# Kernel optimization log

Measured on AMD Instinct MI355X. Metric: run time of the kernel, lower is better.

The kernel has to match this reference:

```python
import jax, jax.numpy as jnp
import numpy as np

HEADS = 7
DIM_HEAD = 64
SCALE = DIM_HEAD ** -0.5


def setup_inputs() -> dict:
    key = jax.random.key(0)
    ks = jax.random.split(key, 6)
    b, n, dim = 8, 1024, 448
    inner = HEADS * DIM_HEAD  # 448
    x = jax.random.normal(ks[0], (b, n, dim), dtype=jnp.float32)
    w_qv = jax.random.normal(ks[1], (dim, 2 * inner), dtype=jnp.float32) * 0.02
    ext_k = jax.random.normal(ks[2], (HEADS, n, DIM_HEAD), dtype=jnp.float32)
    ext_bias = jax.random.normal(ks[3], (HEADS, n, n), dtype=jnp.float32)
    w_out = jax.random.normal(ks[4], (inner, dim), dtype=jnp.float32) * 0.02
    b_out = jnp.zeros((dim,), dtype=jnp.float32)
    return {"x": x, "w_qv": w_qv, "ext_k": ext_k, "ext_bias": ext_bias,
            "w_out": w_out, "b_out": b_out}


def reference(x, w_qv, ext_k, ext_bias, w_out, b_out):
    b, n, dim = x.shape
    qv = x @ w_qv                                   # [b, n, 2*inner]
    q, v = jnp.split(qv, 2, axis=-1)
    # b n (h d) -> b h n d
    q = q.reshape(b, n, HEADS, DIM_HEAD).transpose(0, 2, 1, 3)
    v = v.reshape(b, n, HEADS, DIM_HEAD).transpose(0, 2, 1, 3)
    # scores vs external learned key, additive bias applied BEFORE scale
    dots = (jnp.einsum('bhnd,hmd->bhnm', q, ext_k) + ext_bias[None]) * SCALE
    attn = jax.nn.softmax(dots, axis=-1)
    out = jnp.einsum('bhnm,bhmd->bhnd', attn, v)
    out = out.transpose(0, 2, 1, 3).reshape(b, n, HEADS * DIM_HEAD)
    return out @ w_out + b_out  # dropout is identity in eval mode
```

## Files before the change

kernel.cpp:

```cpp
#include <hip/hip_runtime.h>
#include <hip/hip_bf16.h>
#include <hip/hip_fp16.h>

#define BATCH 8
#define NSEQ 1024
#define DIMM 448
#define NHEAD 7
#define HDIM 64
#define MROWS (BATCH*NSEQ)
#define KDIM 448
#define SCALE_F 0.125f

typedef short short8 __attribute__((ext_vector_type(8)));
typedef float floatx16 __attribute__((ext_vector_type(16)));

#define MFMA32(a,b,c) __builtin_amdgcn_mfma_f32_32x32x16_bf16(a,b,c,0,0,0)

__device__ __forceinline__ unsigned short f2bf(float f){
    __hip_bfloat16 h = __float2bfloat16(f);
    return *reinterpret_cast<unsigned short*>(&h);
}
__device__ __forceinline__ float bf2f(unsigned short u){
    __hip_bfloat16 h; *reinterpret_cast<unsigned short*>(&h) = u;
    return __bfloat162float(h);
}
__device__ __forceinline__ float h2f(unsigned short u){
    __half h; *reinterpret_cast<unsigned short*>(&h) = u;
    return __half2float(h);
}
__device__ __forceinline__ unsigned short f2h(float f){
    __half h = __float2half(f);
    return *reinterpret_cast<unsigned short*>(&h);
}

__global__ __launch_bounds__(256)
void prep_all(const float* __restrict__ x, const float* __restrict__ ek,
              const float* __restrict__ wqv, const float* __restrict__ wout,
              const float* __restrict__ eb,
              unsigned short* __restrict__ xh, unsigned short* __restrict__ ekh,
              unsigned short* __restrict__ wqvTh, unsigned short* __restrict__ woTh,
              unsigned short* __restrict__ woTl, unsigned short* __restrict__ bp)
{
    __shared__ float T[2][64][33];
    const int bx = blockIdx.x, tid = threadIdx.x;

    if (bx < 3584) {
        int i = bx*256 + tid;
        float4 v = ((const float4*)x)[i];
        ((ushort4*)xh)[i] = make_ushort4(f2bf(v.x), f2bf(v.y), f2bf(v.z), f2bf(v.w));
    } else if (bx < 4032) {
        int i = (bx-3584)*256 + tid;
        float4 v = ((const float4*)ek)[i];
        ((ushort4*)ekh)[i] = make_ushort4(f2bf(v.x), f2bf(v.y), f2bf(v.z), f2bf(v.w));
    } else if (bx < 4228) {
        int lid = (bx-4032)*4 + (tid>>6);
        int kc = lid % 56, ng = lid / 56;
        int n = ng*64 + (tid&63);
        unsigned short h[8];
#pragma unroll
        for (int j = 0; j < 8; ++j) h[j] = f2bf(wqv[(size_t)(kc*8+j)*896 + n]);
        size_t o = (size_t)n*KDIM + kc*8;
        *(ushort4*)(wqvTh + o)     = make_ushort4(h[0],h[1],h[2],h[3]);
        *(ushort4*)(wqvTh + o + 4) = make_ushort4(h[4],h[5],h[6],h[7]);
    } else if (bx < 4340) {
        int lid = (bx-4228)*4 + (tid>>6);
        int kc = lid % 56, ng = lid / 56;
        int n = ng*64 + (tid&63);
        ushort4 h0={0,0,0,0}, h1={0,0,0,0}, l0={0,0,0,0}, l1={0,0,0,0};
        if (n < DIMM) {
            unsigned short h[8], l[8];
#pragma unroll
            for (int j = 0; j < 8; ++j) {
                float f = wout[(size_t)(kc*8+j)*DIMM + n];
                h[j] = f2bf(f); l[j] = f2bf(f - bf2f(h[j]));
            }
            h0 = make_ushort4(h[0],h[1],h[2],h[3]); h1 = make_ushort4(h[4],h[5],h[6],h[7]);
            l0 = make_ushort4(l[0],l[1],l[2],l[3]); l1 = make_ushort4(l[4],l[5],l[6],l[7]);
        }
        size_t o = (size_t)n*KDIM + kc*8;
        *(ushort4*)(woTh + o) = h0; *(ushort4*)(woTh + o + 4) = h1;
        *(ushort4*)(woTl + o) = l0; *(ushort4*)(woTl + o + 4) = l1;
    } else {
        const int sub = tid >> 7, st = tid & 127;
        const int lid = (bx-4340)*2 + sub;
        const int mt = lid & 31, qt = (lid>>5) & 15, h = lid >> 9;
#pragma unroll
        for (int it = 0; it < 4; ++it) {
            int idx = it*128 + st;
            int row = idx >> 3, c4 = (idx & 7)*4;
            float4 v = *(const float4*)(eb + ((size_t)(h*NSEQ + qt*64 + row))*NSEQ + mt*32 + c4);
            T[sub][row][c4+0]=v.x; T[sub][row][c4+1]=v.y;
            T[sub][row][c4+2]=v.z; T[sub][row][c4+3]=v.w;
        }
        __syncthreads();
        const int g2 = st >> 6, lane = st & 63;
        const int lq = lane & 31, quad = lane >> 5;
        const int q = g2*32 + lq;
        unsigned short* dst = bp + ((((size_t)h*16 + qt)*32 + mt)*4 + g2*2)*512 + lane*8;
#pragma unroll
        for (int jj = 0; jj < 2; ++jj) {
            unsigned short o[8];
#pragma unroll
            for (int t = 0; t < 8; ++t) {
                int m = (t&3) + 8*(t>>2) + 16*jj + 4*quad;
                o[t] = f2h(T[sub][q][m] * SCALE_F);
            }
            *(ushort4*)(dst + jj*512)     = make_ushort4(o[0],o[1],o[2],o[3]);
            *(ushort4*)(dst + jj*512 + 4) = make_ushort4(o[4],o[5],o[6],o[7]);
        }
    }
}

__global__ __launch_bounds__(64, 2)
void gemm1_reg(const unsigned short* __restrict__ Ah, const unsigned short* __restrict__ Bh,
               unsigned short* __restrict__ qd, unsigned short* __restrict__ vTd)
{
    const int lane = threadIdx.x;
    const int lq = lane & 31, lh = lane >> 5;
    const int m0 = blockIdx.x * 64;
    const int y  = blockIdx.y;
    const int n0 = y * 64;
    const unsigned short* aB = Ah + (size_t)(m0 + lq)*KDIM + lh*8;
    const unsigned short* bB = Bh + (size_t)(n0 + lq)*KDIM + lh*8;

    floatx16 acc[2][2] = {};
    short8 aR[2][2][2], bR[2][2][2];
#define LD1(kt, par) {                                                        \
    _Pragma("unroll") for (int fm = 0; fm < 2; ++fm)                          \
    _Pragma("unroll") for (int c = 0; c < 2; ++c) {                           \
        aR[par][fm][c] = *(const short8*)(aB + (size_t)fm*32*KDIM + (kt)*32 + c*16); \
        bR[par][fm][c] = *(const short8*)(bB + (size_t)fm*32*KDIM + (kt)*32 + c*16); } }

    LD1(0, 0)
#pragma unroll
    for (int kt = 0; kt < 14; ++kt) {
        const int par = kt & 1;
        if (kt < 13) LD1(kt+1, par^1)
#pragma unroll
        for (int c = 0; c < 2; ++c)
#pragma unroll
            for (int fm = 0; fm < 2; ++fm)
#pragma unroll
                for (int fn = 0; fn < 2; ++fn)
                    acc[fm][fn] = MFMA32(aR[par][fm][c], bR[par][fn][c], acc[fm][fn]);
    }
#undef LD1

    if (y < NHEAD) {
#pragma unroll
        for (int fm = 0; fm < 2; ++fm)
#pragma unroll
            for (int fn = 0; fn < 2; ++fn) {
                const int d = fn*32 + lq;
#pragma unroll
                for (int r = 0; r < 16; ++r) {
                    const int gm = m0 + fm*32 + (r&3) + 8*(r>>2) + 4*lh;
                    const int b = gm >> 10, ns = gm & 1023;
                    qd[((size_t)((b*NHEAD + y)*NSEQ + ns))*HDIM + d] = f2bf(acc[fm][fn][r]);
                }
            }
    } else {
        const int head = y - NHEAD;
#pragma unroll
        for (int fm = 0; fm < 2; ++fm)
#pragma unroll
            for (int fn = 0; fn < 2; ++fn) {
                const int d = fn*32 + lq;
#pragma unroll
                for (int r = 0; r < 16; ++r) {
                    const int gm = m0 + fm*32 + (r&3) + 8*(r>>2) + 4*lh;
                    const int b = gm >> 10, ns = gm & 1023;
                    vTd[((size_t)((b*NHEAD + head)*HDIM + d))*NSEQ + ns] = f2bf(acc[fm][fn][r]);
                }
            }
    }
}

__global__ __launch_bounds__(64, 2)
void attn5(const unsigned short* __restrict__ qh_g, const unsigned short* __restrict__ vTh,
           const unsigned short* __restrict__ ekh, const unsigned short* __restrict__ bp,
           unsigned short* __restrict__ aoh, unsigned short* __restrict__ aol)
{
    __shared__ unsigned short pS[1024];
    __shared__ float linv[32];

    const int lane = threadIdx.x;
    const int lq = lane & 31, lh = lane >> 5;
    const int qt2 = blockIdx.x;
    const int qt = qt2 >> 1, g2 = qt2 & 1;
    const int head = blockIdx.y, b = blockIdx.z;
    const int bh = b*NHEAD + head;

    short8 qf[4];
#pragma unroll
    for (int c = 0; c < 4; ++c)
        qf[c] = *(const short8*)(qh_g +
            ((size_t)(bh*NSEQ) + qt2*32 + lq)*HDIM + c*16 + lh*8);

    const unsigned short* kB = ekh + ((size_t)head*NSEQ + lq)*HDIM + lh*8;
    const unsigned short* vB = vTh + ((size_t)(bh*HDIM) + lq)*NSEQ;
    const unsigned short* bB = bp + ((size_t)(head*16 + qt))*65536 + g2*1024 + lane*8;

    short8 kR[2][4], vR[2][4], bR[2][2];
#define PREF(J, par) { const int mm = ((J) < 32) ? (J) : 0;                    \
    _Pragma("unroll") for (int c = 0; c < 4; ++c)                              \
        kR[par][c] = *(const short8*)(kB + (size_t)mm*2048 + c*16);            \
    _Pragma("unroll") for (int c2 = 0; c2 < 2; ++c2)                           \
    _Pragma("unroll") for (int h2 = 0; h2 < 2; ++h2)                           \
        vR[par][c2*2+h2] = *(const short8*)(vB + (size_t)(h2*32)*NSEQ + mm*32 + (c2*2+lh)*8); \
    _Pragma("unroll") for (int u = 0; u < 2; ++u)                              \
        bR[par][u] = *(const short8*)(bB + ((size_t)mm*4 + u)*512); }

    floatx16 O[2] = {};
    float ls = 0.f;

#define SEC(J, par, nxt) {                                                     \
    PREF((J)+1, nxt)                                                           \
    floatx16 S = {};                                                           \
    _Pragma("unroll") for (int c = 0; c < 4; ++c)                              \
        S = MFMA32(kR[par][c], qf[c], S);                                      \
    _Pragma("unroll") for (int g = 0; g < 4; ++g) {                            \
        unsigned short hb[4];                                                  \
        _Pragma("unroll") for (int j2 = 0; j2 < 4; ++j2) {                     \
            const int i = g*4 + j2;                                            \
            float bs = h2f((unsigned short)bR[par][i>>3][i&7]);                \
            float pv = __expf(fmaf(S[i], SCALE_F, bs));                        \
            ls += pv;  hb[j2] = f2bf(pv);                                      \
        }                                                                      \
        *(ushort4*)(pS + g*256 + lq*8 + lh*4) = make_ushort4(hb[0],hb[1],hb[2],hb[3]); \
    }                                                                          \
    _Pragma("unroll") for (int c2 = 0; c2 < 2; ++c2) {                         \
        short8 pf = *(const short8*)(pS + ((c2*2+lh)*32 + lq)*8);              \
        O[0] = MFMA32(pf, vR[par][c2*2+0], O[0]);                              \
        O[1] = MFMA32(pf, vR[par][c2*2+1], O[1]);                              \
    } }

    PREF(0, 0)
    for (int jj = 0; jj < 16; ++jj) {
        SEC(2*jj,   0, 1)
        SEC(2*jj+1, 1, 0)
    }
#undef SEC
#undef PREF

    float lt = ls + __shfl_xor(ls, 32);
    if (lh == 0) linv[lq] = 1.f/lt;

#pragma unroll
    for (int r = 0; r < 16; ++r) {
        const int qr = (r&3) + 8*(r>>2) + 4*lh;
        const float inv = linv[qr];
        const size_t o = ((size_t)(b*NSEQ) + qt2*32 + qr)*DIMM + head*HDIM + lq;
        float v0 = O[0][r]*inv, v1 = O[1][r]*inv;
        unsigned short h0 = f2bf(v0), h1 = f2bf(v1);
        aoh[o]      = h0;  aol[o]      = f2bf(v0 - bf2f(h0));
        aoh[o + 32] = h1;  aol[o + 32] = f2bf(v1 - bf2f(h1));
    }
}

__global__ __launch_bounds__(64, 2)
void gemm2_reg(const unsigned short* __restrict__ Ah, const unsigned short* __restrict__ Al,
               const unsigned short* __restrict__ Bh, const unsigned short* __restrict__ Bl,
               const float* __restrict__ bias, float* __restrict__ out)
{
    const int lane = threadIdx.x;
    const int lq = lane & 31, lh = lane >> 5;
    const int m0 = blockIdx.x * 64;
    const int n0 = blockIdx.y * 64;
    const unsigned short* aBh = Ah + (size_t)(m0 + lq)*KDIM + lh*8;
    const unsigned short* aBl = Al + (size_t)(m0 + lq)*KDIM + lh*8;
    const unsigned short* bBh = Bh + (size_t)(n0 + lq)*KDIM + lh*8;
    const unsigned short* bBl = Bl + (size_t)(n0 + lq)*KDIM + lh*8;

    floatx16 acc[2][2] = {};
    short8 aH[2][2][2], aL[2][2][2], bH[2][2][2], bL[2][2][2];
#define LD2(kt, par) {                                                        \
    _Pragma("unroll") for (int fm = 0; fm < 2; ++fm)                          \
    _Pragma("unroll") for (int c = 0; c < 2; ++c) {                           \
        const size_t off = (size_t)fm*32*KDIM + (kt)*32 + c*16;               \
        aH[par][fm][c] = *(const short8*)(aBh + off);                         \
        aL[par][fm][c] = *(const short8*)(aBl + off);                         \
        bH[par][fm][c] = *(const short8*)(bBh + off);                         \
        bL[par][fm][c] = *(const short8*)(bBl + off); } }

    LD2(0, 0)
#pragma unroll
    for (int kt = 0; kt < 14; ++kt) {
        const int par = kt & 1;
        if (kt < 13) LD2(kt+1, par^1)
#pragma unroll
        for (int c = 0; c < 2; ++c)
#pragma unroll
            for (int fm = 0; fm < 2; ++fm)
#pragma unroll
                for (int fn = 0; fn < 2; ++fn) {
                    acc[fm][fn] = MFMA32(aH[par][fm][c], bH[par][fn][c], acc[fm][fn]);
                    acc[fm][fn] = MFMA32(aL[par][fm][c], bH[par][fn][c], acc[fm][fn]);
                    acc[fm][fn] = MFMA32(aH[par][fm][c], bL[par][fn][c], acc[fm][fn]);
                }
    }
#undef LD2

#pragma unroll
    for (int fm = 0; fm < 2; ++fm)
#pragma unroll
        for (int fn = 0; fn < 2; ++fn) {
            const int gn = n0 + fn*32 + lq;
            const float bv = bias[gn];
#pragma unroll
            for (int r = 0; r < 16; ++r) {
                const int gm = m0 + fm*32 + (r&3) + 8*(r>>2) + 4*lh;
                out[(size_t)gm*DIMM + gn] = acc[fm][fn][r] + bv;
            }
        }
}

extern "C" void kernel_launch(void* const* d_in, const int* in_sizes, int n_in,
                              void* d_out, int out_size, void* d_ws, size_t ws_size,
                              hipStream_t stream)
{
    const float* x    = (const float*)d_in[0];
    const float* wqv  = (const float*)d_in[1];
    const float* ek   = (const float*)d_in[2];
    const float* eb   = (const float*)d_in[3];
    const float* wout = (const float*)d_in[4];
    const float* bout = (const float*)d_in[5];
    float* out = (float*)d_out;

    const size_t MK = (size_t)MROWS*KDIM;
    const size_t EK = (size_t)NHEAD*NSEQ*HDIM;
    unsigned short* p = (unsigned short*)d_ws;
    unsigned short* xh    = p;  p += MK;
    unsigned short* wqvTh = p;  p += (size_t)896*KDIM;
    unsigned short* woTh  = p;  p += (size_t)512*KDIM;
    unsigned short* woTl  = p;  p += (size_t)512*KDIM;
    unsigned short* ekh   = p;  p += EK;
    unsigned short* qh    = p;  p += MK;
    unsigned short* vTh   = p;  p += MK;
    unsigned short* bp    = p;  p += (size_t)NHEAD*NSEQ*NSEQ;
    unsigned short* aoh   = p;  p += MK;
    unsigned short* aol   = p;  p += MK;

    prep_all<<<6132, 256, 0, stream>>>(x, ek, wqv, wout, eb,
                                       xh, ekh, wqvTh, woTh, woTl, bp);
    gemm1_reg<<<dim3(128, 14), 64, 0, stream>>>(xh, wqvTh, qh, vTh);
    attn5<<<dim3(32, NHEAD, BATCH), 64, 0, stream>>>(qh, vTh, ekh, bp, aoh, aol);
    gemm2_reg<<<dim3(128, 7), 64, 0, stream>>>(aoh, aol, woTh, woTl, bout, out);
}
```

Measured before the change: 221.1 us.

## Fold scale and log2e into Q and bias, use fp32 bias as MFMA init

Prescales Q and the external bias by scale*log2(e) so scores feed exp2 directly, and stores the bias in fp32 in MFMA fragment layout so it seeds the score accumulator instead of being added per element. The attention kernel becomes 4-wave blocks, one wave per batch sharing a head and query tile, with a swizzled block order so the bias tile is reused across batches in cache. This removes the per-element fp16 decode and FMA, but doubles the bias storage and read bandwidth.

```diff
diff --git a/kernel.cpp b/kernel.cpp
--- a/kernel.cpp
+++ b/kernel.cpp
@@ -10,6 +10,7 @@
 #define MROWS (BATCH*NSEQ)
 #define KDIM 448
 #define SCALE_F 0.125f
+#define QB_SC 0.18033688011112042f
 
 typedef short short8 __attribute__((ext_vector_type(8)));
 typedef float floatx16 __attribute__((ext_vector_type(16)));
@@ -23,14 +24,6 @@
 __device__ __forceinline__ float bf2f(unsigned short u){
     __hip_bfloat16 h; *reinterpret_cast<unsigned short*>(&h) = u;
     return __bfloat162float(h);
-}
-__device__ __forceinline__ float h2f(unsigned short u){
-    __half h; *reinterpret_cast<unsigned short*>(&h) = u;
-    return __half2float(h);
-}
-__device__ __forceinline__ unsigned short f2h(float f){
-    __half h = __float2half(f);
-    return *reinterpret_cast<unsigned short*>(&h);
 }
 
 __global__ __launch_bounds__(256)
@@ -39,9 +32,9 @@
               const float* __restrict__ eb,
               unsigned short* __restrict__ xh, unsigned short* __restrict__ ekh,
               unsigned short* __restrict__ wqvTh, unsigned short* __restrict__ woTh,
-              unsigned short* __restrict__ woTl, unsigned short* __restrict__ bp)
-{
-    __shared__ float T[2][64][33];
+              unsigned short* __restrict__ woTl, float* __restrict__ bp32)
+{
+    __shared__ float T[4][32][33];
     const int bx = blockIdx.x, tid = threadIdx.x;
 
     if (bx < 3584) {
@@ -81,33 +74,29 @@
         *(ushort4*)(woTh + o) = h0; *(ushort4*)(woTh + o + 4) = h1;
         *(ushort4*)(woTl + o) = l0; *(ushort4*)(woTl + o + 4) = l1;
     } else {
-        const int sub = tid >> 7, st = tid & 127;
-        const int lid = (bx-4340)*2 + sub;
-        const int mt = lid & 31, qt = (lid>>5) & 15, h = lid >> 9;
-#pragma unroll
-        for (int it = 0; it < 4; ++it) {
-            int idx = it*128 + st;
-            int row = idx >> 3, c4 = (idx & 7)*4;
-            float4 v = *(const float4*)(eb + ((size_t)(h*NSEQ + qt*64 + row))*NSEQ + mt*32 + c4);
-            T[sub][row][c4+0]=v.x; T[sub][row][c4+1]=v.y;
-            T[sub][row][c4+2]=v.z; T[sub][row][c4+3]=v.w;
+        const int su = tid >> 6, lane = tid & 63;
+        const int lid = (bx-4340)*4 + su;
+        const int mt = lid & 31, qt2 = (lid>>5) & 31, h = lid >> 10;
+        const int qr = lane >> 1, hf = lane & 1;
+        const float* src = eb + ((size_t)(h*NSEQ) + qt2*32 + qr)*NSEQ + mt*32 + hf*16;
+#pragma unroll
+        for (int j = 0; j < 4; ++j) {
+            float4 v = *(const float4*)(src + j*4);
+            T[su][qr][hf*16 + j*4+0] = v.x;  T[su][qr][hf*16 + j*4+1] = v.y;
+            T[su][qr][hf*16 + j*4+2] = v.z;  T[su][qr][hf*16 + j*4+3] = v.w;
         }
         __syncthreads();
-        const int g2 = st >> 6, lane = st & 63;
         const int lq = lane & 31, quad = lane >> 5;
-        const int q = g2*32 + lq;
-        unsigned short* dst = bp + ((((size_t)h*16 + qt)*32 + mt)*4 + g2*2)*512 + lane*8;
-#pragma unroll
-        for (int jj = 0; jj < 2; ++jj) {
-            unsigned short o[8];
-#pragma unroll
-            for (int t = 0; t < 8; ++t) {
-                int m = (t&3) + 8*(t>>2) + 16*jj + 4*quad;
-                o[t] = f2h(T[sub][q][m] * SCALE_F);
-            }
-            *(ushort4*)(dst + jj*512)     = make_ushort4(o[0],o[1],o[2],o[3]);
-            *(ushort4*)(dst + jj*512 + 4) = make_ushort4(o[4],o[5],o[6],o[7]);
+        float* dst = bp32 + ((size_t)((h*32 + qt2)*32 + mt))*1024 + lane*16;
+        float o[16];
+#pragma unroll
+        for (int r = 0; r < 16; ++r) {
+            const int m = (r&3) + 8*(r>>2) + 4*quad;
+            o[r] = T[su][lq][m] * QB_SC;
         }
+#pragma unroll
+        for (int u = 0; u < 4; ++u)
+            *(float4*)(dst + u*4) = make_float4(o[u*4],o[u*4+1],o[u*4+2],o[u*4+3]);
     }
 }
 
@@ -156,7 +145,7 @@
                 for (int r = 0; r < 16; ++r) {
                     const int gm = m0 + fm*32 + (r&3) + 8*(r>>2) + 4*lh;
                     const int b = gm >> 10, ns = gm & 1023;
-                    qd[((size_t)((b*NHEAD + y)*NSEQ + ns))*HDIM + d] = f2bf(acc[fm][fn][r]);
+                    qd[((size_t)((b*NHEAD + y)*NSEQ + ns))*HDIM + d] = f2bf(acc[fm][fn][r] * QB_SC);
                 }
             }
     } else {
@@ -176,19 +165,22 @@
     }
 }
 
-__global__ __launch_bounds__(64, 2)
-void attn5(const unsigned short* __restrict__ qh_g, const unsigned short* __restrict__ vTh,
-           const unsigned short* __restrict__ ekh, const unsigned short* __restrict__ bp,
+__global__ __launch_bounds__(256, 2)
+void attn8(const unsigned short* __restrict__ qh_g, const unsigned short* __restrict__ vTh,
+           const unsigned short* __restrict__ ekh, const float* __restrict__ bp32,
            unsigned short* __restrict__ aoh, unsigned short* __restrict__ aol)
 {
-    __shared__ unsigned short pS[1024];
-    __shared__ float linv[32];
-
-    const int lane = threadIdx.x;
+    __shared__ unsigned short pS[4][1024];
+    __shared__ float linv[4][32];
+
+    const int tid = threadIdx.x;
+    const int w = tid >> 6, lane = tid & 63;
     const int lq = lane & 31, lh = lane >> 5;
-    const int qt2 = blockIdx.x;
-    const int qt = qt2 >> 1, g2 = qt2 & 1;
-    const int head = blockIdx.y, b = blockIdx.z;
+
+    const int orig = blockIdx.x;
+    const int wg = (orig & 7)*56 + (orig >> 3);
+    const int bq = wg & 1, qt2 = (wg >> 1) & 31, head = wg >> 6;
+    const int b = bq*4 + w;
     const int bh = b*NHEAD + head;
 
     short8 qf[4];
@@ -199,38 +191,42 @@
 
     const unsigned short* kB = ekh + ((size_t)head*NSEQ + lq)*HDIM + lh*8;
     const unsigned short* vB = vTh + ((size_t)(bh*HDIM) + lq)*NSEQ;
-    const unsigned short* bB = bp + ((size_t)(head*16 + qt))*65536 + g2*1024 + lane*8;
-
-    short8 kR[2][4], vR[2][4], bR[2][2];
+    const float* bB = bp32 + ((size_t)(head*32 + qt2))*32768 + lane*16;
+
+    short8 kR[2][4], vR[2][4];
+    float4 bR[2][4];
 #define PREF(J, par) { const int mm = ((J) < 32) ? (J) : 0;                    \
     _Pragma("unroll") for (int c = 0; c < 4; ++c)                              \
         kR[par][c] = *(const short8*)(kB + (size_t)mm*2048 + c*16);            \
     _Pragma("unroll") for (int c2 = 0; c2 < 2; ++c2)                           \
     _Pragma("unroll") for (int h2 = 0; h2 < 2; ++h2)                           \
         vR[par][c2*2+h2] = *(const short8*)(vB + (size_t)(h2*32)*NSEQ + mm*32 + (c2*2+lh)*8); \
-    _Pragma("unroll") for (int u = 0; u < 2; ++u)                              \
-        bR[par][u] = *(const short8*)(bB + ((size_t)mm*4 + u)*512); }
+    _Pragma("unroll") for (int u = 0; u < 4; ++u)                              \
+        bR[par][u] = *(const float4*)(bB + (size_t)mm*1024 + u*4); }
 
     floatx16 O[2] = {};
     float ls = 0.f;
 
 #define SEC(J, par, nxt) {                                                     \
     PREF((J)+1, nxt)                                                           \
-    floatx16 S = {};                                                           \
+    floatx16 S;                                                                \
+    _Pragma("unroll") for (int u = 0; u < 4; ++u) {                            \
+        S[u*4+0] = bR[par][u].x; S[u*4+1] = bR[par][u].y;                      \
+        S[u*4+2] = bR[par][u].z; S[u*4+3] = bR[par][u].w;                      \
+    }                                                                          \
     _Pragma("unroll") for (int c = 0; c < 4; ++c)                              \
         S = MFMA32(kR[par][c], qf[c], S);                                      \
     _Pragma("unroll") for (int g = 0; g < 4; ++g) {                            \
         unsigned short hb[4];                                                  \
         _Pragma("unroll") for (int j2 = 0; j2 < 4; ++j2) {                     \
             const int i = g*4 + j2;                                            \
-            float bs = h2f((unsigned short)bR[par][i>>3][i&7]);                \
-            float pv = __expf(fmaf(S[i], SCALE_F, bs));                        \
+            float pv = __builtin_amdgcn_exp2f(S[i]);                           \
             ls += pv;  hb[j2] = f2bf(pv);                                      \
         }                                                                      \
-        *(ushort4*)(pS + g*256 + lq*8 + lh*4) = make_ushort4(hb[0],hb[1],hb[2],hb[3]); \
+        *(ushort4*)(pS[w] + g*256 + lq*8 + lh*4) = make_ushort4(hb[0],hb[1],hb[2],hb[3]); \
     }                                                                          \
     _Pragma("unroll") for (int c2 = 0; c2 < 2; ++c2) {                         \
-        short8 pf = *(const short8*)(pS + ((c2*2+lh)*32 + lq)*8);              \
+        short8 pf = *(const short8*)(pS[w] + ((c2*2+lh)*32 + lq)*8);           \
         O[0] = MFMA32(pf, vR[par][c2*2+0], O[0]);                              \
         O[1] = MFMA32(pf, vR[par][c2*2+1], O[1]);                              \
     } }
@@ -244,12 +240,12 @@
 #undef PREF
 
     float lt = ls + __shfl_xor(ls, 32);
-    if (lh == 0) linv[lq] = 1.f/lt;
+    if (lh == 0) linv[w][lq] = 1.f/lt;
 
 #pragma unroll
     for (int r = 0; r < 16; ++r) {
         const int qr = (r&3) + 8*(r>>2) + 4*lh;
-        const float inv = linv[qr];
+        const float inv = linv[w][qr];
         const size_t o = ((size_t)(b*NSEQ) + qt2*32 + qr)*DIMM + head*HDIM + lq;
         float v0 = O[0][r]*inv, v1 = O[1][r]*inv;
         unsigned short h0 = f2bf(v0), h1 = f2bf(v1);
@@ -337,13 +333,13 @@
     unsigned short* ekh   = p;  p += EK;
     unsigned short* qh    = p;  p += MK;
     unsigned short* vTh   = p;  p += MK;
-    unsigned short* bp    = p;  p += (size_t)NHEAD*NSEQ*NSEQ;
+    float* bp32 = (float*)p;    p += (size_t)2*NHEAD*NSEQ*NSEQ;
     unsigned short* aoh   = p;  p += MK;
     unsigned short* aol   = p;  p += MK;
 
     prep_all<<<6132, 256, 0, stream>>>(x, ek, wqv, wout, eb,
-                                       xh, ekh, wqvTh, woTh, woTl, bp);
+                                       xh, ekh, wqvTh, woTh, woTl, bp32);
     gemm1_reg<<<dim3(128, 14), 64, 0, stream>>>(xh, wqvTh, qh, vTh);
-    attn5<<<dim3(32, NHEAD, BATCH), 64, 0, stream>>>(qh, vTh, ekh, bp, aoh, aol);
+    attn8<<<448, 256, 0, stream>>>(qh, vTh, ekh, bp32, aoh, aol);
     gemm2_reg<<<dim3(128, 7), 64, 0, stream>>>(aoh, aol, woTh, woTl, bout, out);
 }
```

After: 241.5 us. +9.2%, slower.
